# Performance work log

Measured on AMD Instinct MI355X. Metric: run time of the kernel, lower is better.

## Reference

```python
import jax, jax.numpy as jnp
import numpy as np

SEQ, BATCH, IN, HID = 1024, 64, 512, 2048


def setup_inputs() -> dict:
    key = jax.random.key(0)
    ks = jax.random.split(key, 7)
    x = jax.random.normal(ks[0], (SEQ, BATCH, IN), dtype=jnp.float32)
    # weight_ih ~ N(0, 0.01) per reset_parameters; bias zeros.
    w_ih0 = 0.01 * jax.random.normal(ks[1], (HID, IN), dtype=jnp.float32)
    w_ih1 = 0.01 * jax.random.normal(ks[2], (HID, HID), dtype=jnp.float32)
    # recurrent weight: diagonal, kept in (-1, 1) for a stable 1024-step scan
    w_hh0 = jax.random.uniform(ks[3], (HID,), dtype=jnp.float32, minval=-1.0, maxval=1.0)
    w_hh1 = jax.random.uniform(ks[4], (HID,), dtype=jnp.float32, minval=-1.0, maxval=1.0)
    b0 = jnp.zeros((HID,), dtype=jnp.float32)
    b1 = jnp.zeros((HID,), dtype=jnp.float32)
    return {"x": x, "w_ih0": w_ih0, "w_hh0": w_hh0, "b0": b0,
            "w_ih1": w_ih1, "w_hh1": w_hh1, "b1": b1}


def _indrnn_layer(x, w_ih, w_hh, b):
    # Batched input projection over all timesteps: [T,B,I] x [H,I] -> [T,B,H]
    pre = jnp.einsum('tbi,hi->tbh', x, w_ih) + b
    h0 = jnp.zeros((x.shape[1], w_hh.shape[0]), dtype=x.dtype)

    def step(h, p):
        h_new = jax.nn.relu(p + w_hh * h)  # elementwise recurrence
        return h_new, h_new

    _, out = jax.lax.scan(step, h0, pre)  # out: [T,B,H]
    return out


def reference(x, w_ih0, w_hh0, b0, w_ih1, w_hh1, b1):
    h = _indrnn_layer(x, w_ih0, w_hh0, b0)
    h = _indrnn_layer(h, w_ih1, w_hh1, b1)
    return h  # [T, B, H] outputs of last layer
```

## Files before the change

### kernel.cpp

```cpp
#include <hip/hip_runtime.h>


#define T_SEQ 1024
#define NB 64
#define NI 512
#define NH 2048
#define BH (NB * NH)
#define M_ROWS (T_SEQ * NB)

typedef _Float16 f16;
typedef __attribute__((ext_vector_type(8))) _Float16 f16x8;
typedef __attribute__((ext_vector_type(4))) _Float16 f16x4;
typedef __attribute__((ext_vector_type(4))) float f32x4;

__device__ __forceinline__ void gload_lds16(const f16* g, const f16* lds) {
  __builtin_amdgcn_global_load_lds(
      (const __attribute__((address_space(1))) unsigned int*)g,
      (__attribute__((address_space(3))) unsigned int*)lds, 16, 0, 0);
}
__device__ __forceinline__ void barrier_raw() {
  __builtin_amdgcn_sched_barrier(0);
  __builtin_amdgcn_s_barrier();
  __builtin_amdgcn_sched_barrier(0);
}
#define LGKM0()                                        \
  do {                                                 \
    asm volatile("s_waitcnt lgkmcnt(0)" ::: "memory"); \
    __builtin_amdgcn_sched_barrier(0);                 \
  } while (0)
#define VMCNT4() asm volatile("s_waitcnt vmcnt(4)" ::: "memory")

__global__ __launch_bounds__(256)
void cvt_f16x4(const float* __restrict__ in, f16* __restrict__ out, int n4) {
  int i = blockIdx.x * blockDim.x + threadIdx.x;
  const int stride = gridDim.x * blockDim.x;
  for (; i < n4; i += stride) {
    f32x4 v = ((const f32x4*)in)[i];
    f16x4 h;
    h[0] = (f16)v[0]; h[1] = (f16)v[1]; h[2] = (f16)v[2]; h[3] = (f16)v[3];
    ((f16x4*)out)[i] = h;
  }
}

template <int K, typename OutT>
__global__ __launch_bounds__(512, 2)
void gemm8(const f16* __restrict__ A, const f16* __restrict__ Bt,
           const float* __restrict__ bias, OutT* __restrict__ C) {
  constexpr int NT = K / 64;
  __shared__ f16 sA[2][2][128 * 64];
  __shared__ f16 sB[2][2][128 * 64];

  const int tid = threadIdx.x, wid = tid >> 6, lane = tid & 63;
  int id = (int)blockIdx.x;
  id = (id & 7) * 256 + (id >> 3);
  const int bn = id & 7, bm = id >> 3;
  const long m0 = (long)bm * 256, n0 = (long)bn * 256;

  const int wr = wid >> 2, wc = wid & 3;
  const int lrow = lane & 15, lk = (lane >> 4) * 8;

  const int xorv = (lrow & 7) << 4;
  const int TxA = (((wr * 16 + lrow) * 128) + lk * 2) ^ xorv;
  const int TxB = (((wc * 16 + lrow) * 128) + lk * 2) ^ xorv;

  auto ldA = [&](int buf, int mt, int ks) -> f16x8 {
    const char* p = (const char*)&sA[buf][mt >> 2][0];
    return *(const f16x8*)(p + (mt & 3) * 4096 + (TxA ^ (ks << 6)));
  };
  auto ldB = [&](int buf, int nt, int ks) -> f16x8 {
    const char* p = (const char*)&sB[buf][nt >> 1][0];
    return *(const f16x8*)(p + (nt & 1) * 8192 + (TxB ^ (ks << 6)));
  };

  const int srow = wid * 8 + (lane >> 3);
  const int scol = ((lane & 7) ^ ((lane >> 3) & 7)) * 8;
  const int ldst = wid * 512;

  auto stageA = [&](int buf, int h, int kt) {
    if (kt >= NT) kt = NT - 1;
    const f16* g = A + (m0 + h * 128 + srow) * (long)K + kt * 64 + scol;
    gload_lds16(g,                &sA[buf][h][ldst]);
    gload_lds16(g + 64 * (long)K, &sA[buf][h][ldst + 4096]);
  };
  auto stageB = [&](int buf, int h, int kt) {
    if (kt >= NT) kt = NT - 1;
    const f16* g = Bt + (n0 + h * 128 + srow) * (long)K + kt * 64 + scol;
    gload_lds16(g,                &sB[buf][h][ldst]);
    gload_lds16(g + 64 * (long)K, &sB[buf][h][ldst + 4096]);
  };

  f32x4 acc[8][4] = {};
  f16x8 aR[4][2], bR[4][2];

#define MFMA16(MBASE, NBASE)                                                   \
  __builtin_amdgcn_s_setprio(1);                                               \
  _Pragma("unroll") for (int mi = 0; mi < 4; ++mi)                             \
      _Pragma("unroll") for (int ni = 0; ni < 2; ++ni)                         \
          _Pragma("unroll") for (int ks = 0; ks < 2; ++ks)                     \
              acc[MBASE + mi][NBASE + ni] =                                    \
                  __builtin_amdgcn_mfma_f32_16x16x32_f16(                      \
                      aR[mi][ks], bR[NBASE + ni][ks],                          \
                      acc[MBASE + mi][NBASE + ni], 0, 0, 0);                   \
  __builtin_amdgcn_s_setprio(0);

  stageA(0, 0, 0);
  stageB(0, 1, 0);
  stageA(0, 1, 0);
  stageB(0, 0, 0);
  stageA(1, 0, 1);
  stageB(1, 1, 1);
  VMCNT4();
  barrier_raw();

  for (int t = 0; t < NT; ++t) {
    const int cur = t & 1, nxt = cur ^ 1;
#pragma unroll
    for (int i = 0; i < 4; ++i) { aR[i][0] = ldA(cur, i, 0); aR[i][1] = ldA(cur, i, 1); }
#pragma unroll
    for (int i = 0; i < 2; ++i) { bR[i][0] = ldB(cur, i, 0); bR[i][1] = ldB(cur, i, 1); }
    stageA(nxt, 1, t + 1);
    barrier_raw();
    LGKM0();
    MFMA16(0, 0);
    barrier_raw();
#pragma unroll
    for (int i = 0; i < 2; ++i) { bR[2 + i][0] = ldB(cur, 2 + i, 0); bR[2 + i][1] = ldB(cur, 2 + i, 1); }
    stageB(nxt, 0, t + 1);
    barrier_raw();
    LGKM0();
    MFMA16(0, 2);
    barrier_raw();
#pragma unroll
    for (int i = 0; i < 4; ++i) { aR[i][0] = ldA(cur, 4 + i, 0); aR[i][1] = ldA(cur, 4 + i, 1); }
    stageA(cur, 0, t + 2);
    barrier_raw();
    LGKM0();
    MFMA16(4, 2);
    barrier_raw();
    stageB(cur, 1, t + 2);
    barrier_raw();
    MFMA16(4, 0);
    VMCNT4();
    barrier_raw();
  }

  float bv[4];
#pragma unroll
  for (int nt = 0; nt < 4; ++nt) bv[nt] = bias[n0 + (4 * nt + wc) * 16 + lrow];
#pragma unroll
  for (int mt = 0; mt < 8; ++mt) {
    const long rbase = m0 + (2 * mt + wr) * 16 + ((lane >> 4) << 2);
#pragma unroll
    for (int j = 0; j < 4; ++j) {
      OutT* cp = C + (rbase + j) * (long)NH + n0 + wc * 16 + lrow;
#pragma unroll
      for (int nt = 0; nt < 4; ++nt)
        cp[nt * 64] = (OutT)(acc[mt][nt][j] + bv[nt]);
    }
  }
#undef MFMA16
}

template <typename PT>
__global__ __launch_bounds__(256)
void scan_inplace(PT* __restrict__ P, const float* __restrict__ w_hh) {
  const int c = blockIdx.x * 256 + threadIdx.x;
  const float w = w_hh[c & (NH - 1)];
  PT* p = P + c;
  float h = 0.f;
  float v0 = (float)p[0L * BH];
  float v1 = (float)p[1L * BH];
  float v2 = (float)p[2L * BH];
  float v3 = (float)p[3L * BH];
  for (int t = 0; t < T_SEQ; t += 4) {
    float n0 = 0.f, n1 = 0.f, n2 = 0.f, n3 = 0.f;
    if (t + 4 < T_SEQ) {
      const PT* q = p + (long)(t + 4) * BH;
      n0 = (float)q[0L * BH];
      n1 = (float)q[1L * BH];
      n2 = (float)q[2L * BH];
      n3 = (float)q[3L * BH];
    }
    h = fmaxf(fmaf(w, h, v0), 0.f); p[(long)(t + 0) * BH] = (PT)h;
    h = fmaxf(fmaf(w, h, v1), 0.f); p[(long)(t + 1) * BH] = (PT)h;
    h = fmaxf(fmaf(w, h, v2), 0.f); p[(long)(t + 2) * BH] = (PT)h;
    h = fmaxf(fmaf(w, h, v3), 0.f); p[(long)(t + 3) * BH] = (PT)h;
    v0 = n0; v1 = n1; v2 = n2; v3 = n3;
  }
}

extern "C" void kernel_launch(void* const* d_in, const int* in_sizes, int n_in,
                              void* d_out, int out_size, void* d_ws, size_t ws_size,
                              hipStream_t stream) {
  const float* x     = (const float*)d_in[0];
  const float* w_ih0 = (const float*)d_in[1];
  const float* w_hh0 = (const float*)d_in[2];
  const float* b0    = (const float*)d_in[3];
  const float* w_ih1 = (const float*)d_in[4];
  const float* w_hh1 = (const float*)d_in[5];
  const float* b1    = (const float*)d_in[6];
  float* out = (float*)d_out;

  char* ws = (char*)d_ws;
  f16* x16   = (f16*)(ws);
  f16* w0_16 = (f16*)(ws + 67108864);
  f16* w1_16 = (f16*)(ws + 69206016);
  f16* P     = (f16*)(ws + 77594624);

  cvt_f16x4<<<2048, 256, 0, stream>>>(x,     x16,   33554432 / 4);
  cvt_f16x4<<<1024, 256, 0, stream>>>(w_ih0, w0_16, 1048576 / 4);
  cvt_f16x4<<<2048, 256, 0, stream>>>(w_ih1, w1_16, 4194304 / 4);

  gemm8<NI, f16><<<2048, 512, 0, stream>>>(x16, w0_16, b0, P);
  scan_inplace<f16><<<BH / 256, 256, 0, stream>>>(P, w_hh0);
  gemm8<NH, float><<<2048, 512, 0, stream>>>(P, w1_16, b1, out);
  scan_inplace<float><<<BH / 256, 256, 0, stream>>>(out, w_hh1);
}
```

Baseline: 1.159 ms.

## Emit layer-2 GEMM output as f16, deepen scan prefetch, fuse conversion kernels

The second GEMM now writes its pre-activations as f16 into a separate workspace buffer, and the final scan reads them and writes fp32 output. This roughly halves the GEMM store and the scan read traffic for layer 2. The three conversion launches are merged into one kernel, and the scan prefetches 8 timesteps instead of 4 for more memory-level parallelism. It adds f16 rounding of the layer-2 pre-activations and needs enough workspace for the new path, falling back to the old fp32 path otherwise.

```diff
diff --git a/kernel.cpp b/kernel.cpp
--- a/kernel.cpp
+++ b/kernel.cpp
@@ -31,14 +31,21 @@
 #define VMCNT4() asm volatile("s_waitcnt vmcnt(4)" ::: "memory")
 
 __global__ __launch_bounds__(256)
-void cvt_f16x4(const float* __restrict__ in, f16* __restrict__ out, int n4) {
-  int i = blockIdx.x * blockDim.x + threadIdx.x;
-  const int stride = gridDim.x * blockDim.x;
-  for (; i < n4; i += stride) {
-    f32x4 v = ((const f32x4*)in)[i];
+void cvt_all(const float* __restrict__ x, const float* __restrict__ w0,
+             const float* __restrict__ w1, f16* __restrict__ x16,
+             f16* __restrict__ w0_16, f16* __restrict__ w1_16) {
+  constexpr int N0 = 33554432 / 4, N1 = 1048576 / 4, N2 = 4194304 / 4;
+  int i = blockIdx.x * 256 + threadIdx.x;
+  const int stride = gridDim.x * 256;
+  for (; i < N0 + N1 + N2; i += stride) {
+    const float* src; f16* dst; int j;
+    if (i < N0)            { src = x;  dst = x16;   j = i; }
+    else if (i < N0 + N1)  { src = w0; dst = w0_16; j = i - N0; }
+    else                   { src = w1; dst = w1_16; j = i - N0 - N1; }
+    f32x4 v = ((const f32x4*)src)[j];
     f16x4 h;
     h[0] = (f16)v[0]; h[1] = (f16)v[1]; h[2] = (f16)v[2]; h[3] = (f16)v[3];
-    ((f16x4*)out)[i] = h;
+    ((f16x4*)dst)[j] = h;
   }
 }
 
@@ -161,31 +168,30 @@
 #undef MFMA16
 }
 
-template <typename PT>
+template <typename InT, typename OutT>
 __global__ __launch_bounds__(256)
-void scan_inplace(PT* __restrict__ P, const float* __restrict__ w_hh) {
+void scan_k(const InT* in, OutT* out, const float* __restrict__ w_hh) {
   const int c = blockIdx.x * 256 + threadIdx.x;
   const float w = w_hh[c & (NH - 1)];
-  PT* p = P + c;
-  float h = 0.f;
-  float v0 = (float)p[0L * BH];
-  float v1 = (float)p[1L * BH];
-  float v2 = (float)p[2L * BH];
-  float v3 = (float)p[3L * BH];
-  for (int t = 0; t < T_SEQ; t += 4) {
-    float n0 = 0.f, n1 = 0.f, n2 = 0.f, n3 = 0.f;
-    if (t + 4 < T_SEQ) {
-      const PT* q = p + (long)(t + 4) * BH;
-      n0 = (float)q[0L * BH];
-      n1 = (float)q[1L * BH];
-      n2 = (float)q[2L * BH];
-      n3 = (float)q[3L * BH];
+  const InT* pi = in + c;
+  OutT* po = out + c;
+  float h = 0.f, v[8], n[8];
+#pragma unroll
+  for (int j = 0; j < 8; ++j) v[j] = (float)pi[(long)j * BH];
+  for (int t = 0; t < T_SEQ; t += 8) {
+    if (t + 8 < T_SEQ) {
+#pragma unroll
+      for (int j = 0; j < 8; ++j) n[j] = (float)pi[(long)(t + 8 + j) * BH];
+    } else {
+#pragma unroll
+      for (int j = 0; j < 8; ++j) n[j] = 0.f;
     }
-    h = fmaxf(fmaf(w, h, v0), 0.f); p[(long)(t + 0) * BH] = (PT)h;
-    h = fmaxf(fmaf(w, h, v1), 0.f); p[(long)(t + 1) * BH] = (PT)h;
-    h = fmaxf(fmaf(w, h, v2), 0.f); p[(long)(t + 2) * BH] = (PT)h;
-    h = fmaxf(fmaf(w, h, v3), 0.f); p[(long)(t + 3) * BH] = (PT)h;
-    v0 = n0; v1 = n1; v2 = n2; v3 = n3;
+#pragma unroll
+    for (int j = 0; j < 8; ++j) {
+      h = fmaxf(fmaf(w, h, v[j]), 0.f);
+      po[(long)(t + j) * BH] = (OutT)h;
+      v[j] = n[j];
+    }
   }
 }
 
@@ -206,13 +212,18 @@
   f16* w0_16 = (f16*)(ws + 67108864);
   f16* w1_16 = (f16*)(ws + 69206016);
   f16* P     = (f16*)(ws + 77594624);
-
-  cvt_f16x4<<<2048, 256, 0, stream>>>(x,     x16,   33554432 / 4);
-  cvt_f16x4<<<1024, 256, 0, stream>>>(w_ih0, w0_16, 1048576 / 4);
-  cvt_f16x4<<<2048, 256, 0, stream>>>(w_ih1, w1_16, 4194304 / 4);
+  f16* P2    = (f16*)(ws + 346030080);
+  const bool p2_f16 = ws_size >= (size_t)346030080 + 268435456;
+
+  cvt_all<<<2048, 256, 0, stream>>>(x, w_ih0, w_ih1, x16, w0_16, w1_16);
 
   gemm8<NI, f16><<<2048, 512, 0, stream>>>(x16, w0_16, b0, P);
-  scan_inplace<f16><<<BH / 256, 256, 0, stream>>>(P, w_hh0);
-  gemm8<NH, float><<<2048, 512, 0, stream>>>(P, w1_16, b1, out);
-  scan_inplace<float><<<BH / 256, 256, 0, stream>>>(out, w_hh1);
-}
+  scan_k<f16, f16><<<BH / 256, 256, 0, stream>>>(P, P, w_hh0);
+  if (p2_f16) {
+    gemm8<NH, f16><<<2048, 512, 0, stream>>>(P, w1_16, b1, P2);
+    scan_k<f16, float><<<BH / 256, 256, 0, stream>>>(P2, out, w_hh1);
+  } else {
+    gemm8<NH, float><<<2048, 512, 0, stream>>>(P, w1_16, b1, out);
+    scan_k<float, float><<<BH / 256, 256, 0, stream>>>(out, out, w_hh1);
+  }
+}
```

Result: faster. 985.1 us (-15.0%).
